# Kernel tuning notes

Hardware: AMD Instinct MI355X
Metric: run time of the kernel (lower is better)

The kernel has to match this reference:

```python
import jax, jax.numpy as jnp
import numpy as np

# Model dims (match init_kwargs)
B, S, HID = 2, 2048, 2048
NH, HD = 16, 128          # num_heads, head_dim (nope dim == rope dim == HD)
QHD = 2 * HD              # q_head_dim = nope + rope
QLR, KVLR = 1536, 512     # q_lora_rank, kv_lora_rank
ROPE_BASE = 10000.0
EPS = 1e-6


def rms_norm(x, w):
    # NOTE: source RMSNorm uses sum (not mean) of squares -- faithful.
    return x * jax.lax.rsqrt(jnp.sum(x * x, axis=-1, keepdims=True) + EPS) * w


def rope_cos_sin(seq_len, dim, base=ROPE_BASE):
    inv_freq = 1.0 / (base ** (jnp.arange(0, dim, 2, dtype=jnp.float32) / dim))
    freqs = jnp.outer(jnp.arange(seq_len, dtype=jnp.float32), inv_freq)  # [S, dim/2]
    emb = jnp.concatenate([freqs, freqs], axis=-1)                        # [S, dim]
    return jnp.cos(emb), jnp.sin(emb)


def rotate_half(x):
    h = x.shape[-1] // 2
    return jnp.concatenate([-x[..., h:], x[..., :h]], axis=-1)


def setup_inputs() -> dict:
    key = jax.random.key(0)
    ks = jax.random.split(key, 9)
    s = 0.02
    return {
        "hidden_states": jax.random.normal(ks[0], (B, S, HID), jnp.float32),
        "attn_mask": jnp.zeros((B, 1, S, S), jnp.float32),
        "q_a_W": jax.random.normal(ks[1], (QLR, HID), jnp.float32) * s,
        "q_a_b": jnp.zeros((QLR,), jnp.float32),
        "q_a_norm_w": jnp.ones((QLR,), jnp.float32),
        "q_b_W": jax.random.normal(ks[2], (NH * QHD, QLR), jnp.float32) * s,
        "kv_a_W": jax.random.normal(ks[3], (KVLR + HD, HID), jnp.float32) * s,
        "kv_b_W": jax.random.normal(ks[4], (KVLR, NH, 2, HD), jnp.float32) * s,
        "o_W": jax.random.normal(ks[5], (HID, NH * HD), jnp.float32) * s,
    }


def reference(hidden_states, attn_mask, q_a_W, q_a_b, q_a_norm_w, q_b_W,
              kv_a_W, kv_b_W, o_W):
    b, s, _ = hidden_states.shape
    # --- low-rank Q path ---
    q_a = hidden_states @ q_a_W.T + q_a_b                      # [b,s,QLR]
    q = rms_norm(q_a, q_a_norm_w) @ q_b_W.T                    # [b,s,NH*QHD]
    q = q.reshape(b, s, NH, QHD).transpose(0, 2, 1, 3)         # [b,h,s,QHD]
    q_nope, q_pe = q[..., :HD], q[..., HD:]
    # --- compressed KV path (MQA-style shared latent) ---
    ckv_full = hidden_states @ kv_a_W.T                        # [b,s,KVLR+HD]
    ckv, k_pe = ckv_full[..., :KVLR], ckv_full[..., KVLR:]     # [b,s,KVLR],[b,s,HD]
    # --- partial RoPE ---
    cos, sin = rope_cos_sin(s, HD)                             # [s,HD]
    cos4, sin4 = cos[None, None], sin[None, None]
    q_pe = q_pe * cos4 + rotate_half(q_pe) * sin4              # [b,h,s,HD]
    k_pe = k_pe * cos[None] + rotate_half(k_pe) * sin[None]    # [b,s,HD]
    # --- absorbed kv_b matrices ---
    q_absorb = kv_b_W[:, :, 0, :]                              # [KVLR,h,HD]
    o_absorb = kv_b_W[:, :, 1, :]                              # [KVLR,h,HD]
    q_lat = jnp.einsum('chd,bhsd->bhsc', q_absorb, q_nope)     # [b,h,s,KVLR]
    scale = 1.0 / np.sqrt(KVLR + HD).astype(np.float32)
    scores = (jnp.einsum('bhsc,btc->bhst', q_lat, ckv)
              + jnp.einsum('bhsd,btd->bhst', q_pe, k_pe)) * scale
    scores = scores + attn_mask                                # [b,h,s,s]
    attn = jax.nn.softmax(scores, axis=-1)
    out = jnp.einsum('bhst,btc->bhsc', attn, ckv)              # [b,h,s,KVLR]
    out = jnp.einsum('bhsc,chd->bhsd', out, o_absorb)          # [b,h,s,HD]
    out = out.transpose(0, 2, 1, 3).reshape(b, s, NH * HD)
    return out @ o_W.T                                         # [b,s,HID]
```

## Files before the change

### kernel.cpp

```cpp
#include <hip/hip_runtime.h>
#include <hip/hip_bf16.h>


using bf16 = __hip_bfloat16;
typedef __attribute__((ext_vector_type(8))) short short8;
typedef __attribute__((ext_vector_type(4))) short short4_t;
typedef __attribute__((ext_vector_type(4))) float f32x4;

__device__ __forceinline__ float b2f(bf16 x) { return __bfloat162float(x); }
__device__ __forceinline__ bf16 f2b(float x) { return __float2bfloat16(x); }

typedef __attribute__((address_space(3))) unsigned lds_u32;
typedef const __attribute__((address_space(1))) unsigned glb_u32;
__device__ __forceinline__ void dma16(const bf16* g, bf16* l) {
  __builtin_amdgcn_global_load_lds((glb_u32*)g, (lds_u32*)l, 16, 0, 0);
}

template<bool RS>
__global__ __launch_bounds__(512, 2) void gemm8(
    const bf16* __restrict__ A, const bf16* __restrict__ B, bf16* __restrict__ C,
    int K, int lda, int ldb, int ldc, long sa, long sb, long sc,
    float cscale, float* __restrict__ rs_out)
{
  __shared__ bf16 As[2][16384];
  __shared__ bf16 Bs[2][16384];

  const int z = blockIdx.z;
  const bf16* Ag = A + (long)z * sa + (long)(blockIdx.x * 256) * lda;
  const bf16* Bg = B + (long)z * sb + (long)(blockIdx.y * 256) * ldb;

  const int m0 = blockIdx.x * 256, n0 = blockIdx.y * 256;
  const int tid = threadIdx.x, lane = tid & 63, wave = tid >> 6;
  const int wm = wave >> 2, wn = wave & 3;
  const int mrow = lane & 15, quad = lane >> 4;
  const int lrow = lane >> 3, lcol = lane & 7;
  const int swg = (lcol ^ lrow) << 3;
  const int sw  = (mrow & 7) << 3;
  const int nt = K >> 6;

  auto stA = [&](int h, int t) {
    if (t < nt) {
      const int b = t & 1;
      const long kk = (long)t * 64 + swg;
      #pragma unroll
      for (int q = 0; q < 2; q++) {
        const int rb = q * 128 + h * 64 + wave * 8;
        dma16(Ag + (long)(rb + lrow) * lda + kk, &As[b][rb * 64]);
      }
    }
  };
  auto stB = [&](int h, int t) {
    if (t < nt) {
      const int b = t & 1;
      const long kk = (long)t * 64 + swg;
      #pragma unroll
      for (int q = 0; q < 2; q++) {
        const int c = q * 8 + wave;
        const int rb = (c >> 2) * 64 + h * 32 + (c & 3) * 8;
        dma16(Bg + (long)(rb + lrow) * ldb + kk, &Bs[b][rb * 64]);
      }
    }
  };

  f32x4 acc[8][4];
  #pragma unroll
  for (int m = 0; m < 8; m++)
    #pragma unroll
    for (int j = 0; j < 4; j++)
      #pragma unroll
      for (int r = 0; r < 4; r++) acc[m][j][r] = 0.0f;

  stA(0, 0); stB(0, 0); stB(1, 0); stA(1, 0);
  stA(0, 1); stB(0, 1); stB(1, 1);
  asm volatile("s_waitcnt vmcnt(6)" ::: "memory");
  __builtin_amdgcn_s_barrier();

  auto group = [&](int bb, int tn1, int tn2, bool lv) {
    const bf16* a0 = &As[bb][(wm * 128 + mrow) * 64];
    const bf16* b0 = &Bs[bb][(wn * 64 + mrow) * 64];
    short8 af[4][2], bf[2][2], ag2[4][2], bg2[2][2];
    #pragma unroll
    for (int m = 0; m < 4; m++)
      #pragma unroll
      for (int ks = 0; ks < 2; ks++)
        af[m][ks] = *(const short8*)&a0[m * 1024 + ((ks * 32 + quad * 8) ^ sw)];
    #pragma unroll
    for (int j = 0; j < 2; j++)
      #pragma unroll
      for (int ks = 0; ks < 2; ks++)
        bf[j][ks] = *(const short8*)&b0[j * 1024 + ((ks * 32 + quad * 8) ^ sw)];
    stA(1, tn1);
    asm volatile("s_waitcnt lgkmcnt(0)" ::: "memory");
    __builtin_amdgcn_s_barrier();
    __builtin_amdgcn_s_setprio(1);
    #pragma unroll
    for (int ks = 0; ks < 2; ks++)
      #pragma unroll
      for (int m = 0; m < 4; m++)
        #pragma unroll
        for (int j = 0; j < 2; j++)
          acc[m][j] = __builtin_amdgcn_mfma_f32_16x16x32_bf16(bf[j][ks], af[m][ks], acc[m][j], 0, 0, 0);
    __builtin_amdgcn_s_setprio(0);
    #pragma unroll
    for (int j = 0; j < 2; j++)
      #pragma unroll
      for (int ks = 0; ks < 2; ks++)
        bg2[j][ks] = *(const short8*)&b0[(2 + j) * 1024 + ((ks * 32 + quad * 8) ^ sw)];
    stA(0, tn2);
    asm volatile("s_waitcnt lgkmcnt(0)" ::: "memory");
    __builtin_amdgcn_s_barrier();
    __builtin_amdgcn_s_setprio(1);
    #pragma unroll
    for (int ks = 0; ks < 2; ks++)
      #pragma unroll
      for (int m = 0; m < 4; m++)
        #pragma unroll
        for (int j = 0; j < 2; j++)
          acc[m][2 + j] = __builtin_amdgcn_mfma_f32_16x16x32_bf16(bg2[j][ks], af[m][ks], acc[m][2 + j], 0, 0, 0);
    __builtin_amdgcn_s_setprio(0);
    #pragma unroll
    for (int m = 0; m < 4; m++)
      #pragma unroll
      for (int ks = 0; ks < 2; ks++)
        ag2[m][ks] = *(const short8*)&a0[(4 + m) * 1024 + ((ks * 32 + quad * 8) ^ sw)];
    stB(0, tn2);
    asm volatile("s_waitcnt lgkmcnt(0)" ::: "memory");
    __builtin_amdgcn_s_barrier();
    __builtin_amdgcn_s_setprio(1);
    #pragma unroll
    for (int ks = 0; ks < 2; ks++)
      #pragma unroll
      for (int m = 0; m < 4; m++)
        #pragma unroll
        for (int j = 0; j < 2; j++)
          acc[4 + m][j] = __builtin_amdgcn_mfma_f32_16x16x32_bf16(bf[j][ks], ag2[m][ks], acc[4 + m][j], 0, 0, 0);
    __builtin_amdgcn_s_setprio(0);
    stB(1, tn2);
    if (lv) asm volatile("s_waitcnt vmcnt(0)" ::: "memory");
    else    asm volatile("s_waitcnt vmcnt(6)" ::: "memory");
    __builtin_amdgcn_s_barrier();
    __builtin_amdgcn_s_setprio(1);
    #pragma unroll
    for (int ks = 0; ks < 2; ks++)
      #pragma unroll
      for (int m = 0; m < 4; m++)
        #pragma unroll
        for (int j = 0; j < 2; j++)
          acc[4 + m][2 + j] = __builtin_amdgcn_mfma_f32_16x16x32_bf16(bg2[j][ks], ag2[m][ks], acc[4 + m][2 + j], 0, 0, 0);
    __builtin_amdgcn_s_setprio(0);
  };

  const int niter = nt >> 1;
  #pragma unroll 1
  for (int i = 0; i < niter; ++i) {
    const int t0 = 2 * i;
    const bool lv = (i == niter - 1);
    group(0, t0 + 1, t0 + 2, lv);
    group(1, t0 + 2, t0 + 3, lv);
  }

  bf16* Cz = C + (long)z * sc;
  float* rs = RS ? rs_out + (long)z * 2048 : nullptr;
  #pragma unroll
  for (int mi = 0; mi < 8; mi++) {
    const int m = m0 + wm * 128 + mi * 16 + mrow;
    const long rowoff = (long)m * ldc;
    float rsum = 0.0f;
    #pragma unroll
    for (int nj = 0; nj < 4; nj++) {
      short4_t p;
      #pragma unroll
      for (int r = 0; r < 4; r++) {
        float v = acc[mi][nj][r] * cscale;
        if (RS) { v = __expf(v); rsum += v; }
        bf16 b = f2b(v); p[r] = *(short*)&b;
      }
      *(short4_t*)&Cz[rowoff + n0 + wn * 64 + nj * 16 + quad * 4] = p;
    }
    if (RS) {
      rsum += __shfl_xor(rsum, 16);
      rsum += __shfl_xor(rsum, 32);
      if (quad == 0) atomicAdd(&rs[m], rsum);
    }
  }
}

template<bool RSIN>
__global__ __launch_bounds__(512, 2) void gemm8n(
    const bf16* __restrict__ A, const bf16* __restrict__ B, bf16* __restrict__ C,
    int K, int lda, int ldb, int ldc, long sa, long sb, long sc,
    const float* __restrict__ rs_in)
{
  __shared__ bf16 As[2][8192];
  __shared__ bf16 Bs[2][16384];

  const int z = blockIdx.z;
  const bf16* Ag = A + (long)z * sa + (long)(blockIdx.x * 128) * lda;
  const bf16* Bg = B + (long)z * sb + (long)(blockIdx.y * 256) * ldb;

  const int m0 = blockIdx.x * 128, n0 = blockIdx.y * 256;
  const int tid = threadIdx.x, lane = tid & 63, wave = tid >> 6;
  const int wm = wave >> 2, wn = wave & 3;
  const int mrow = lane & 15, quad = lane >> 4;
  const int lrow = lane >> 3, lcol = lane & 7;
  const int swg = (lcol ^ lrow) << 3;
  const int sw  = (mrow & 7) << 3;
  const int nt = K >> 6;

  auto stA = [&](int h, int t) {
    if (t < nt) {
      const int b = t & 1;
      const long kk = (long)t * 64 + swg;
      const int rb = h * 64 + wave * 8;
      dma16(Ag + (long)(rb + lrow) * lda + kk, &As[b][rb * 64]);
    }
  };
  auto stB = [&](int h, int t) {
    if (t < nt) {
      const int b = t & 1;
      const long kk = (long)t * 64 + swg;
      #pragma unroll
      for (int q = 0; q < 2; q++) {
        const int rb = h * 128 + q * 64 + wave * 8;
        dma16(Bg + (long)(rb + lrow) * ldb + kk, &Bs[b][rb * 64]);
      }
    }
  };

  f32x4 acc[4][4];
  #pragma unroll
  for (int m = 0; m < 4; m++)
    #pragma unroll
    for (int j = 0; j < 4; j++)
      #pragma unroll
      for (int r = 0; r < 4; r++) acc[m][j][r] = 0.0f;

  stB(0, 0); stB(1, 0); stA(0, 0); stA(1, 0);
  stA(0, 1); stA(1, 1); stB(0, 1); stB(1, 1);
  asm volatile("s_waitcnt vmcnt(6)" ::: "memory");
  __builtin_amdgcn_s_barrier();

  #pragma unroll 1
  for (int t = 0; t < nt; ++t) {
    const int bb = t & 1;
    const bf16* a0 = &As[bb][(wm * 64 + mrow) * 64];
    const bf16* b0 = &Bs[bb][(wn * 64 + mrow) * 64];
    short8 af[2][2], ag[2][2], bf[4][2];
    #pragma unroll
    for (int m = 0; m < 2; m++)
      #pragma unroll
      for (int ks = 0; ks < 2; ks++)
        af[m][ks] = *(const short8*)&a0[m * 1024 + ((ks * 32 + quad * 8) ^ sw)];
    #pragma unroll
    for (int j = 0; j < 4; j++)
      #pragma unroll
      for (int ks = 0; ks < 2; ks++)
        bf[j][ks] = *(const short8*)&b0[j * 1024 + ((ks * 32 + quad * 8) ^ sw)];
    asm volatile("s_waitcnt lgkmcnt(0)" ::: "memory");
    __builtin_amdgcn_s_barrier();
    stB(0, t + 2); stB(1, t + 2);
    __builtin_amdgcn_s_setprio(1);
    #pragma unroll
    for (int ks = 0; ks < 2; ks++)
      #pragma unroll
      for (int m = 0; m < 2; m++)
        #pragma unroll
        for (int j = 0; j < 4; j++)
          acc[m][j] = __builtin_amdgcn_mfma_f32_16x16x32_bf16(bf[j][ks], af[m][ks], acc[m][j], 0, 0, 0);
    __builtin_amdgcn_s_setprio(0);
    #pragma unroll
    for (int m = 0; m < 2; m++)
      #pragma unroll
      for (int ks = 0; ks < 2; ks++)
        ag[m][ks] = *(const short8*)&a0[(2 + m) * 1024 + ((ks * 32 + quad * 8) ^ sw)];
    asm volatile("s_waitcnt lgkmcnt(0)" ::: "memory");
    if (t >= nt - 2) asm volatile("s_waitcnt vmcnt(0)" ::: "memory");
    else             asm volatile("s_waitcnt vmcnt(4)" ::: "memory");
    __builtin_amdgcn_s_barrier();
    stA(0, t + 2); stA(1, t + 2);
    __builtin_amdgcn_s_setprio(1);
    #pragma unroll
    for (int ks = 0; ks < 2; ks++)
      #pragma unroll
      for (int m = 0; m < 2; m++)
        #pragma unroll
        for (int j = 0; j < 4; j++)
          acc[2 + m][j] = __builtin_amdgcn_mfma_f32_16x16x32_bf16(bf[j][ks], ag[m][ks], acc[2 + m][j], 0, 0, 0);
    __builtin_amdgcn_s_setprio(0);
  }

  bf16* Cz = C + (long)z * sc;
  #pragma unroll
  for (int mi = 0; mi < 4; mi++) {
    const int m = m0 + wm * 64 + mi * 16 + mrow;
    const long rowoff = (long)m * ldc;
    float rsc = 1.0f;
    if (RSIN) rsc = 1.0f / rs_in[(long)z * 2048 + m];
    #pragma unroll
    for (int nj = 0; nj < 4; nj++) {
      short4_t p;
      #pragma unroll
      for (int r = 0; r < 4; r++) {
        float v = acc[mi][nj][r] * rsc;
        bf16 b = f2b(v); p[r] = *(short*)&b;
      }
      *(short4_t*)&Cz[rowoff + n0 + wn * 64 + nj * 16 + quad * 4] = p;
    }
  }
}

template<int TM, bool OUT_BF16>
__global__ __launch_bounds__(256, 2) void gemm_bt(
    const bf16* __restrict__ A, const bf16* __restrict__ B, void* __restrict__ Cv,
    int M, int N, int K, int lda, int ldb, int ldc,
    long sa0, long sa1, long sb0, long sb1, long sc0, long sc1, int zdiv,
    float cscale, void* __restrict__ Cv2, int nsplit, int ldc2,
    float* __restrict__ rs_out, const float* __restrict__ rs_in)
{
  __shared__ bf16 As[TM * 64];
  __shared__ bf16 Bs[128 * 64];
  constexpr int WJ = (TM == 256) ? 8 : 4;

  const int z = blockIdx.z, z0 = z / zdiv, z1 = z % zdiv;
  A += z0 * sa0 + z1 * sa1;
  B += z0 * sb0 + z1 * sb1;
  const long coff = z0 * sc0 + z1 * sc1;

  const int m0 = blockIdx.x * TM, n0 = blockIdx.y * 128;
  const int tid = threadIdx.x, lane = tid & 63, wave = tid >> 6;
  const int wm = (TM == 256) ? wave * 64 : (wave & 1) * 64;
  const int wn = (TM == 256) ? 0 : (wave >> 1) * 64;
  const int mrow = lane & 15, quad = lane >> 4;
  const int srow = tid >> 2, scol = (tid & 3) * 8;

  f32x4 acc[WJ][4];
  #pragma unroll
  for (int j = 0; j < WJ; j++)
    #pragma unroll
    for (int i = 0; i < 4; i++)
      #pragma unroll
      for (int r = 0; r < 4; r++) acc[j][i][r] = 0.0f;

  const bf16* ag = A + (long)(m0 + srow) * lda + scol;
  const bf16* bg = B + (long)(n0 + srow) * ldb + scol;
  bf16* as_ = As + wave * 512;
  bf16* bs_ = Bs + wave * 512;

  for (int k0 = 0; k0 < K; k0 += 64) {
    __syncthreads();
    #pragma unroll
    for (int g = 0; g < TM / 64; g++) {
      dma16(ag + k0 + (long)(g * 64) * lda,      as_ + g * 2048);
      dma16(ag + k0 + 32 + (long)(g * 64) * lda, as_ + TM * 32 + g * 2048);
    }
    dma16(bg + k0,                  bs_);
    dma16(bg + k0 + 64l * ldb,      bs_ + 2048);
    dma16(bg + k0 + 32,             bs_ + 4096);
    dma16(bg + k0 + 32 + 64l * ldb, bs_ + 6144);
    __syncthreads();

    #pragma unroll
    for (int h = 0; h < 2; h++) {
      short8 af[4], bfr[WJ];
      #pragma unroll
      for (int i = 0; i < 4; i++)
        af[i] = *(const short8*)&As[h * (TM * 32) + (wm + i * 16 + mrow) * 32 + quad * 8];
      #pragma unroll
      for (int j = 0; j < WJ; j++)
        bfr[j] = *(const short8*)&Bs[h * 4096 + (wn + j * 16 + mrow) * 32 + quad * 8];
      #pragma unroll
      for (int j = 0; j < WJ; j++)
        #pragma unroll
        for (int i = 0; i < 4; i++)
          acc[j][i] = __builtin_amdgcn_mfma_f32_16x16x32_bf16(bfr[j], af[i], acc[j][i], 0, 0, 0);
    }
  }

  if (OUT_BF16) {
    const bool use2 = (Cv2 != nullptr) && (n0 >= nsplit);
    bf16* Cb  = use2 ? (bf16*)Cv2 : (bf16*)Cv + coff;
    const int ldcb = use2 ? ldc2 : ldc;
    const int nb0  = use2 ? (n0 - nsplit) : n0;
    #pragma unroll
    for (int i = 0; i < 4; i++) {
      const int m = m0 + wm + i * 16 + mrow;
      const long rowoff = (long)m * ldcb;
      float rsc = 1.0f;
      if (rs_in) rsc = 1.0f / rs_in[(long)z * 2048 + m];
      float rsum = 0.0f;
      #pragma unroll
      for (int j = 0; j < WJ; j++) {
        short4_t p;
        #pragma unroll
        for (int r = 0; r < 4; r++) {
          float v = acc[j][i][r] * cscale;
          if (rs_out) { v = __expf(v); rsum += v; }
          v *= rsc;
          bf16 b = f2b(v); p[r] = *(short*)&b;
        }
        *(short4_t*)&Cb[rowoff + nb0 + wn + j * 16 + quad * 4] = p;
      }
      if (rs_out) {
        rsum += __shfl_xor(rsum, 16);
        rsum += __shfl_xor(rsum, 32);
        if (quad == 0) atomicAdd(&rs_out[(long)z * 2048 + m], rsum);
      }
    }
  } else {
    float* C = (float*)Cv + coff;
    #pragma unroll
    for (int i = 0; i < 4; i++) {
      const long rowoff = (long)(m0 + wm + i * 16 + mrow) * ldc;
      #pragma unroll
      for (int j = 0; j < WJ; j++) {
        f32x4 p;
        #pragma unroll
        for (int r = 0; r < 4; r++) p[r] = acc[j][i][r] * cscale;
        *(f32x4*)&C[rowoff + n0 + wn + j * 16 + quad * 4] = p;
      }
    }
  }
}


__global__ __launch_bounds__(256) void cvt4_kernel(const float* __restrict__ in,
                                                   bf16* __restrict__ out, long n4)
{
  long i = (long)blockIdx.x * 256 + threadIdx.x;
  if (i < n4) {
    f32x4 v = *(const f32x4*)(in + i * 4);
    short4_t p;
    #pragma unroll
    for (int r = 0; r < 4; r++) { bf16 b = f2b(v[r]); p[r] = *(short*)&b; }
    *(short4_t*)(out + i * 4) = p;
  }
}

__global__ __launch_bounds__(256) void cvtW_kernel(
    const float* __restrict__ qaW, const float* __restrict__ qbW,
    const float* __restrict__ kvaW, const float* __restrict__ kvbW,
    const float* __restrict__ oW,
    bf16* __restrict__ qaWB, bf16* __restrict__ qbWB, bf16* __restrict__ kvaWB,
    bf16* __restrict__ kvbWB, bf16* __restrict__ oWB)
{
  long i = (long)blockIdx.x * 256 + threadIdx.x;
  const float* src; bf16* dst; long o;
  if (i < 786432)           { src = qaW;  dst = qaWB;  o = i; }
  else if (i < 2359296)     { src = qbW;  dst = qbWB;  o = i - 786432; }
  else if (i < 2686976)     { src = kvaW; dst = kvaWB; o = i - 2359296; }
  else if (i < 3211264)     { src = kvbW; dst = kvbWB; o = i - 2686976; }
  else                      { src = oW;   dst = oWB;   o = i - 3211264; }
  f32x4 v = *(const f32x4*)(src + o * 4);
  short4_t p;
  #pragma unroll
  for (int r = 0; r < 4; r++) { bf16 b = f2b(v[r]); p[r] = *(short*)&b; }
  *(short4_t*)(dst + o * 4) = p;
}

__global__ __launch_bounds__(256) void oabsT_kernel(const float* __restrict__ kvb,
                                                    bf16* __restrict__ oT)
{
  long idx = (long)blockIdx.x * 256 + threadIdx.x;
  int c = (int)(idx & 511);
  long r = idx >> 9;
  int d = (int)(r & 127);
  int h = (int)(r >> 7);
  oT[idx] = f2b(kvb[(long)c * 4096 + h * 256 + 128 + d]);
}

__global__ __launch_bounds__(256) void rmsnorm_kernel(const bf16* __restrict__ qa,
                                                      const float* __restrict__ bias,
                                                      const float* __restrict__ w,
                                                      bf16* __restrict__ out)
{
  const int s = blockIdx.x;
  const int tid = threadIdx.x, lane = tid & 63, wave = tid >> 6;
  const bf16* row = qa + (long)s * 1536;
  float v[6]; float ss = 0.f;
  #pragma unroll
  for (int i = 0; i < 6; i++) {
    int t = tid + i * 256;
    v[i] = b2f(row[t]) + bias[t];
    ss += v[i] * v[i];
  }
  #pragma unroll
  for (int off = 32; off; off >>= 1) ss += __shfl_xor(ss, off);
  __shared__ float red[4];
  if (lane == 0) red[wave] = ss;
  __syncthreads();
  ss = red[0] + red[1] + red[2] + red[3];
  float rs = rsqrtf(ss + 1e-6f);
  bf16* orow = out + (long)s * 1536;
  #pragma unroll
  for (int i = 0; i < 6; i++) {
    int t = tid + i * 256;
    orow[t] = f2b(v[i] * rs * w[t]);
  }
}

__global__ __launch_bounds__(256) void rope_q_kernel(const bf16* __restrict__ q,
                                                     bf16* __restrict__ Q640)
{
  long idx = (long)blockIdx.x * 256 + threadIdx.x;
  int d = (int)(idx & 63);
  long r = idx >> 6;
  int s = (int)(r & 2047);
  long bh = r >> 11;
  int h = (int)(bh & 15);
  long b = bh >> 4;
  const bf16* qrow = q + (b * 2048 + s) * 4096l + h * 256 + 128;
  float x1 = b2f(qrow[d]), x2 = b2f(qrow[d + 64]);
  float ang = (float)s * powf(10000.0f, -(float)d * (1.0f / 64.0f));
  float sn, cs; sincosf(ang, &sn, &cs);
  bf16* orow = Q640 + (bh * 2048 + s) * 640 + 512;
  orow[d]      = f2b(x1 * cs - x2 * sn);
  orow[d + 64] = f2b(x2 * cs + x1 * sn);
}

__global__ __launch_bounds__(256) void rope_k_kernel(bf16* __restrict__ ckv)
{
  long idx = (long)blockIdx.x * 256 + threadIdx.x;
  int d = (int)(idx & 63);
  long r = idx >> 6;
  int t = (int)(r & 2047);
  bf16* row = ckv + r * 640 + 512;
  float x1 = b2f(row[d]), x2 = b2f(row[d + 64]);
  float ang = (float)t * powf(10000.0f, -(float)d * (1.0f / 64.0f));
  float sn, cs; sincosf(ang, &sn, &cs);
  row[d]      = f2b(x1 * cs - x2 * sn);
  row[d + 64] = f2b(x2 * cs + x1 * sn);
}

__global__ __launch_bounds__(256) void ckvT_kernel(const bf16* __restrict__ ckv,
                                                   bf16* __restrict__ ckvT)
{
  long idx = (long)blockIdx.x * 256 + threadIdx.x;
  int t = (int)(idx & 2047);
  long r = idx >> 11;
  int c = (int)(r & 511);
  long b = r >> 9;
  ckvT[idx] = ckv[(b * 2048 + t) * 640 + c];
}


extern "C" void kernel_launch(void* const* d_in, const int* in_sizes, int n_in,
                              void* d_out, int out_size, void* d_ws, size_t ws_size,
                              hipStream_t stream)
{
  const float* hidden = (const float*)d_in[0];
  const float* mask   = (const float*)d_in[1];
  const float* qaW    = (const float*)d_in[2];
  const float* qab    = (const float*)d_in[3];
  const float* qanw   = (const float*)d_in[4];
  const float* qbW    = (const float*)d_in[5];
  const float* kvaW   = (const float*)d_in[6];
  const float* kvbW   = (const float*)d_in[7];
  const float* oW     = (const float*)d_in[8];
  float* out = (float*)d_out;
  (void)in_sizes; (void)n_in; (void)out_size; (void)mask;

  char* ws = (char*)d_ws;
  if (ws_size < 144179200u) return;

  const bool big = (ws_size >= 177733632u);
  const int CH = big ? 8 : 4;
  const int nchunk = big ? 4 : 8;

  bf16* Q640    = (bf16*)(ws + 0);
  bf16* qa      = (bf16*)(ws + 0);
  bf16* hiddenB = (bf16*)(ws + 25165824);
  bf16* qan     = (bf16*)(ws + 41943040);
  bf16* qaWB    = (bf16*)(ws + 54525952);
  bf16* kvaWB   = (bf16*)(ws + 60817408);
  bf16* qbWB    = (bf16*)(ws + 63438848);
  bf16* qB       = (bf16*)(ws + 83886080);
  bf16* Sbuf     = (bf16*)(ws + 83886080);
  bf16* attn_out = (bf16*)(ws + 83886080);
  const long tail = big ? 150994944l : 117440512l;
  bf16* ckv     = (bf16*)(ws + tail);
  bf16* ckvT    = (bf16*)(ws + tail + 5242880);
  float* rowsum = (float*)(ws + tail + 9437184);
  bf16* kvbWB   = (bf16*)(ws + tail + 12058624);
  bf16* oWB     = (bf16*)(ws + tail + 16252928);
  bf16* oabsT   = (bf16*)(ws + tail + 24641536);

  cvt4_kernel<<<dim3(8192), 256, 0, stream>>>(hidden, hiddenB, 2097152l);
  cvtW_kernel<<<dim3(16640), 256, 0, stream>>>(qaW, qbW, kvaW, kvbW, oW,
                                               qaWB, qbWB, kvaWB, kvbWB, oWB);
  oabsT_kernel<<<dim3(4096), 256, 0, stream>>>(kvbW, oabsT);

  gemm_bt<128, true><<<dim3(32, 17, 1), 256, 0, stream>>>(hiddenB, qaWB, qa,
      4096, 2176, 2048, 2048, 2048, 1536, 0, 0, 0, 0, 0, 0, 1, 1.0f,
      ckv, 1536, 640, nullptr, nullptr);
  rmsnorm_kernel<<<dim3(4096), 256, 0, stream>>>(qa, qab, qanw, qan);

  gemm8<false><<<dim3(16, 16, 1), 512, 0, stream>>>(qan, qbWB, qB,
      1536, 1536, 1536, 4096, 0l, 0l, 0l, 1.0f, nullptr);

  rope_k_kernel<<<dim3(1024), 256, 0, stream>>>(ckv);
  rope_q_kernel<<<dim3(16384), 256, 0, stream>>>(qB, Q640);
  ckvT_kernel<<<dim3(8192), 256, 0, stream>>>(ckv, ckvT);

  gemm_bt<128, true><<<dim3(16, 4, 32), 256, 0, stream>>>(qB, kvbWB, Q640,
      2048, 512, 128, 4096, 4096, 640,
      256l, 8388608l, 256l, 0l, 1310720l, 20971520l, 2, 1.0f,
      nullptr, 0, 0, nullptr, nullptr);

  hipMemsetAsync(rowsum, 0, 262144, stream);
  const float scale = 1.0f / sqrtf(640.0f);
  for (int c = 0; c < nchunk; ++c) {
    int b = (c * CH) >> 4;
    bf16* Qchunk = Q640 + (long)c * CH * 1310720;
    float* rsc = rowsum + (long)c * CH * 2048;
    gemm8<true><<<dim3(8, 8, CH), 512, 0, stream>>>(Qchunk, ckv + (long)b * 1310720, Sbuf,
        640, 640, 640, 2048, 1310720l, 0l, 4194304l, scale, rsc);
    gemm8n<true><<<dim3(16, 2, CH), 512, 0, stream>>>(Sbuf, ckvT + (long)b * 1048576, Qchunk,
        2048, 2048, 2048, 640, 4194304l, 0l, 1310720l, rsc);
  }

  gemm_bt<128, true><<<dim3(16, 1, 32), 256, 0, stream>>>(Q640, oabsT, attn_out,
      2048, 128, 512, 640, 512, 2048,
      1310720l, 20971520l, 65536l, 0l, 128l, 4194304l, 2, 1.0f,
      nullptr, 0, 0, nullptr, nullptr);

  gemm_bt<128, false><<<dim3(32, 16, 1), 256, 0, stream>>>(attn_out, oWB, out,
      4096, 2048, 2048, 2048, 2048, 2048, 0, 0, 0, 0, 0, 0, 1, 1.0f,
      nullptr, 0, 0, nullptr, nullptr);
}
```

Baseline: 767.7 us.

## Switch gemm8 to 32x32x16 MFMA tiles with fewer barrier phases

Replaces the 16x16x32 bf16 MFMA tiling in gemm8 with 32x32x16 MFMA instructions, so each wave holds 4x2 accumulators of 16 floats and loads wider fragments per k-step. The LDS read pattern and swizzle offsets are recomputed for the 32-row layout. Each group shrinks from four barrier-separated compute phases to two, and the A and B prefetches are issued together. The intent is better MFMA throughput and fewer LDS reads and barriers, at the cost of less interleaving between loads and compute and a new epilogue mapping that must match the 32x32 output layout.

New measurement: 806.3 us. 5.0% more time.

```diff
diff --git a/kernel.cpp b/kernel.cpp
--- a/kernel.cpp
+++ b/kernel.cpp
@@ -6,6 +6,7 @@
 typedef __attribute__((ext_vector_type(8))) short short8;
 typedef __attribute__((ext_vector_type(4))) short short4_t;
 typedef __attribute__((ext_vector_type(4))) float f32x4;
+typedef __attribute__((ext_vector_type(16))) float f32x16;
 
 __device__ __forceinline__ float b2f(bf16 x) { return __bfloat162float(x); }
 __device__ __forceinline__ bf16 f2b(float x) { return __float2bfloat16(x); }
@@ -32,11 +33,14 @@
   const int m0 = blockIdx.x * 256, n0 = blockIdx.y * 256;
   const int tid = threadIdx.x, lane = tid & 63, wave = tid >> 6;
   const int wm = wave >> 2, wn = wave & 3;
-  const int mrow = lane & 15, quad = lane >> 4;
+  const int l31 = lane & 31, hi = lane >> 5;
   const int lrow = lane >> 3, lcol = lane & 7;
   const int swg = (lcol ^ lrow) << 3;
-  const int sw  = (mrow & 7) << 3;
   const int nt = K >> 6;
+
+  int fc[4];
+  #pragma unroll
+  for (int ks = 0; ks < 4; ks++) fc[ks] = (((ks * 2 + hi) ^ (lane & 7)) << 3);
 
   auto stA = [&](int h, int t) {
     if (t < nt) {
@@ -62,13 +66,13 @@
     }
   };
 
-  f32x4 acc[8][4];
-  #pragma unroll
-  for (int m = 0; m < 8; m++)
-    #pragma unroll
-    for (int j = 0; j < 4; j++)
-      #pragma unroll
-      for (int r = 0; r < 4; r++) acc[m][j][r] = 0.0f;
+  f32x16 acc[4][2];
+  #pragma unroll
+  for (int m = 0; m < 4; m++)
+    #pragma unroll
+    for (int j = 0; j < 2; j++)
+      #pragma unroll
+      for (int r = 0; r < 16; r++) acc[m][j][r] = 0.0f;
 
   stA(0, 0); stB(0, 0); stB(1, 0); stA(1, 0);
   stA(0, 1); stB(0, 1); stB(1, 1);
@@ -76,77 +80,49 @@
   __builtin_amdgcn_s_barrier();
 
   auto group = [&](int bb, int tn1, int tn2, bool lv) {
-    const bf16* a0 = &As[bb][(wm * 128 + mrow) * 64];
-    const bf16* b0 = &Bs[bb][(wn * 64 + mrow) * 64];
-    short8 af[4][2], bf[2][2], ag2[4][2], bg2[2][2];
-    #pragma unroll
-    for (int m = 0; m < 4; m++)
-      #pragma unroll
-      for (int ks = 0; ks < 2; ks++)
-        af[m][ks] = *(const short8*)&a0[m * 1024 + ((ks * 32 + quad * 8) ^ sw)];
-    #pragma unroll
-    for (int j = 0; j < 2; j++)
-      #pragma unroll
-      for (int ks = 0; ks < 2; ks++)
-        bf[j][ks] = *(const short8*)&b0[j * 1024 + ((ks * 32 + quad * 8) ^ sw)];
+    const bf16* a0 = &As[bb][(wm * 128 + l31) * 64];
+    const bf16* b0 = &Bs[bb][(wn * 64 + l31) * 64];
+    short8 af[2][4], ag2[2][4], bf[4], bg2[4];
+    #pragma unroll
+    for (int mi = 0; mi < 2; mi++)
+      #pragma unroll
+      for (int ks = 0; ks < 4; ks++)
+        af[mi][ks] = *(const short8*)&a0[mi * 2048 + fc[ks]];
+    #pragma unroll
+    for (int ks = 0; ks < 4; ks++) {
+      bf[ks]  = *(const short8*)&b0[fc[ks]];
+      bg2[ks] = *(const short8*)&b0[2048 + fc[ks]];
+    }
     stA(1, tn1);
     asm volatile("s_waitcnt lgkmcnt(0)" ::: "memory");
     __builtin_amdgcn_s_barrier();
     __builtin_amdgcn_s_setprio(1);
     #pragma unroll
-    for (int ks = 0; ks < 2; ks++)
-      #pragma unroll
-      for (int m = 0; m < 4; m++)
-        #pragma unroll
-        for (int j = 0; j < 2; j++)
-          acc[m][j] = __builtin_amdgcn_mfma_f32_16x16x32_bf16(bf[j][ks], af[m][ks], acc[m][j], 0, 0, 0);
+    for (int ks = 0; ks < 4; ks++)
+      #pragma unroll
+      for (int mi = 0; mi < 2; mi++) {
+        acc[mi][0] = __builtin_amdgcn_mfma_f32_32x32x16_bf16(bf[ks],  af[mi][ks], acc[mi][0], 0, 0, 0);
+        acc[mi][1] = __builtin_amdgcn_mfma_f32_32x32x16_bf16(bg2[ks], af[mi][ks], acc[mi][1], 0, 0, 0);
+      }
     __builtin_amdgcn_s_setprio(0);
     #pragma unroll
-    for (int j = 0; j < 2; j++)
-      #pragma unroll
-      for (int ks = 0; ks < 2; ks++)
-        bg2[j][ks] = *(const short8*)&b0[(2 + j) * 1024 + ((ks * 32 + quad * 8) ^ sw)];
-    stA(0, tn2);
+    for (int mi = 0; mi < 2; mi++)
+      #pragma unroll
+      for (int ks = 0; ks < 4; ks++)
+        ag2[mi][ks] = *(const short8*)&a0[(2 + mi) * 2048 + fc[ks]];
+    stA(0, tn2); stB(0, tn2); stB(1, tn2);
     asm volatile("s_waitcnt lgkmcnt(0)" ::: "memory");
-    __builtin_amdgcn_s_barrier();
-    __builtin_amdgcn_s_setprio(1);
-    #pragma unroll
-    for (int ks = 0; ks < 2; ks++)
-      #pragma unroll
-      for (int m = 0; m < 4; m++)
-        #pragma unroll
-        for (int j = 0; j < 2; j++)
-          acc[m][2 + j] = __builtin_amdgcn_mfma_f32_16x16x32_bf16(bg2[j][ks], af[m][ks], acc[m][2 + j], 0, 0, 0);
-    __builtin_amdgcn_s_setprio(0);
-    #pragma unroll
-    for (int m = 0; m < 4; m++)
-      #pragma unroll
-      for (int ks = 0; ks < 2; ks++)
-        ag2[m][ks] = *(const short8*)&a0[(4 + m) * 1024 + ((ks * 32 + quad * 8) ^ sw)];
-    stB(0, tn2);
-    asm volatile("s_waitcnt lgkmcnt(0)" ::: "memory");
-    __builtin_amdgcn_s_barrier();
-    __builtin_amdgcn_s_setprio(1);
-    #pragma unroll
-    for (int ks = 0; ks < 2; ks++)
-      #pragma unroll
-      for (int m = 0; m < 4; m++)
-        #pragma unroll
-        for (int j = 0; j < 2; j++)
-          acc[4 + m][j] = __builtin_amdgcn_mfma_f32_16x16x32_bf16(bf[j][ks], ag2[m][ks], acc[4 + m][j], 0, 0, 0);
-    __builtin_amdgcn_s_setprio(0);
-    stB(1, tn2);
     if (lv) asm volatile("s_waitcnt vmcnt(0)" ::: "memory");
     else    asm volatile("s_waitcnt vmcnt(6)" ::: "memory");
     __builtin_amdgcn_s_barrier();
     __builtin_amdgcn_s_setprio(1);
     #pragma unroll
-    for (int ks = 0; ks < 2; ks++)
-      #pragma unroll
-      for (int m = 0; m < 4; m++)
-        #pragma unroll
-        for (int j = 0; j < 2; j++)
-          acc[4 + m][2 + j] = __builtin_amdgcn_mfma_f32_16x16x32_bf16(bg2[j][ks], ag2[m][ks], acc[4 + m][2 + j], 0, 0, 0);
+    for (int ks = 0; ks < 4; ks++)
+      #pragma unroll
+      for (int mi = 0; mi < 2; mi++) {
+        acc[2 + mi][0] = __builtin_amdgcn_mfma_f32_32x32x16_bf16(bf[ks],  ag2[mi][ks], acc[2 + mi][0], 0, 0, 0);
+        acc[2 + mi][1] = __builtin_amdgcn_mfma_f32_32x32x16_bf16(bg2[ks], ag2[mi][ks], acc[2 + mi][1], 0, 0, 0);
+      }
     __builtin_amdgcn_s_setprio(0);
   };
 
@@ -162,25 +138,26 @@
   bf16* Cz = C + (long)z * sc;
   float* rs = RS ? rs_out + (long)z * 2048 : nullptr;
   #pragma unroll
-  for (int mi = 0; mi < 8; mi++) {
-    const int m = m0 + wm * 128 + mi * 16 + mrow;
+  for (int mi = 0; mi < 4; mi++) {
+    const int m = m0 + wm * 128 + mi * 32 + l31;
     const long rowoff = (long)m * ldc;
     float rsum = 0.0f;
     #pragma unroll
-    for (int nj = 0; nj < 4; nj++) {
-      short4_t p;
-      #pragma unroll
-      for (int r = 0; r < 4; r++) {
-        float v = acc[mi][nj][r] * cscale;
-        if (RS) { v = __expf(v); rsum += v; }
-        bf16 b = f2b(v); p[r] = *(short*)&b;
-      }
-      *(short4_t*)&Cz[rowoff + n0 + wn * 64 + nj * 16 + quad * 4] = p;
-    }
+    for (int nj = 0; nj < 2; nj++)
+      #pragma unroll
+      for (int rg = 0; rg < 4; rg++) {
+        short4_t p;
+        #pragma unroll
+        for (int rr = 0; rr < 4; rr++) {
+          float v = acc[mi][nj][rg * 4 + rr] * cscale;
+          if (RS) { v = __expf(v); rsum += v; }
+          bf16 b = f2b(v); p[rr] = *(short*)&b;
+        }
+        *(short4_t*)&Cz[rowoff + n0 + wn * 64 + nj * 32 + rg * 8 + hi * 4] = p;
+      }
     if (RS) {
-      rsum += __shfl_xor(rsum, 16);
       rsum += __shfl_xor(rsum, 32);
-      if (quad == 0) atomicAdd(&rs[m], rsum);
+      if (hi == 0) atomicAdd(&rs[m], rsum);
     }
   }
 }
```
